# Performance work log

Measured on AMD Instinct MI355X. Metric: run time of the kernel, lower is better.

The kernel has to match this reference:

```python
import jax, jax.numpy as jnp
import numpy as np

B, HT, WD, DIM = 8, 128, 128, 512
NUM_HEADS = 8
HEAD_DIM = DIM // NUM_HEADS
K = 7  # kernel_size
R = K // 2


def setup_inputs() -> dict:
    key = jax.random.key(0)
    k1, k2 = jax.random.split(key)
    x = jax.random.normal(k1, (B, HT, WD, DIM), dtype=jnp.float32)
    # nn.Linear(dim, 2*dim, bias=False); stored as [in, out] so y = x @ W_qk
    W_qk = jax.random.normal(k2, (DIM, 2 * DIM), dtype=jnp.float32) * (DIM ** -0.5)
    return {"x": x, "W_qk": W_qk}


def reference(x, W_qk):
    Bsz, H, W, C = x.shape
    scale = HEAD_DIM ** -0.5
    # qk projection -> [B,H,W,2,heads,head_dim]
    qk = (x @ W_qk).reshape(Bsz, H, W, 2, NUM_HEADS, HEAD_DIM)
    q = qk[..., 0, :, :] * scale          # [B,H,W,hd,d]
    kk = qk[..., 1, :, :]                 # [B,H,W,hd,d]
    # NATTEN border handling: window start clamped so the KxK window stays inside.
    starts_i = jnp.clip(jnp.arange(H) - R, 0, H - K)  # [H]
    starts_j = jnp.clip(jnp.arange(W) - R, 0, W - K)  # [W]
    attn = []
    for ki in range(K):
        k_row = kk[:, starts_i + ki]          # [B,H,W,hd,d] (gather rows)
        for kj in range(K):
            k_n = k_row[:, :, starts_j + kj]  # [B,H,W,hd,d] (gather cols)
            attn.append(jnp.einsum('bhwnd,bhwnd->bhwn', q, k_n))
    attn = jnp.stack(attn, axis=-1)           # [B,H,W,hd,K*K]
    return jnp.transpose(attn, (0, 3, 1, 2, 4))  # [B,hd,H,W,K*K]
```

## Files before the change

### kernel.cpp

```cpp
#include <hip/hip_runtime.h>

typedef __attribute__((ext_vector_type(8))) short short8;
typedef __attribute__((ext_vector_type(4))) float floatx4;

__device__ __forceinline__ unsigned short f2bf(float f) {
  union { float f; unsigned u; } x; x.f = f;
  unsigned u = x.u + 0x7fffu + ((x.u >> 16) & 1u);
  return (unsigned short)(u >> 16);
}

__device__ __forceinline__ void gload_lds16(const void* g, void* l) {
  __builtin_amdgcn_global_load_lds(
      (const __attribute__((address_space(1))) unsigned int*)g,
      (__attribute__((address_space(3))) unsigned int*)l, 16, 0, 0);
}


__global__ __launch_bounds__(256) void cvt_x(const float4* __restrict__ x,
                                             uint2* __restrict__ o) {
  size_t idx = (size_t)blockIdx.x * 256 + threadIdx.x;
  float4 v = x[idx];
  uint2 r;
  r.x = (unsigned)f2bf(v.x) | ((unsigned)f2bf(v.y) << 16);
  r.y = (unsigned)f2bf(v.z) | ((unsigned)f2bf(v.w) << 16);
  o[idx] = r;
}

__global__ __launch_bounds__(256) void cvt_w(const float* __restrict__ w,
                                             unsigned short* __restrict__ wt) {
  int tid = blockIdx.x * 256 + threadIdx.x;
  int n = tid >> 9, k = tid & 511;
  float v = w[k * 1024 + n];
  if (n < 512) v *= 0.125f;
  wt[tid] = f2bf(v);
}

__global__ __launch_bounds__(512, 2) void gemm_bt(const unsigned short* __restrict__ A,
                                                  const unsigned short* __restrict__ Bt,
                                                  unsigned short* __restrict__ C) {
  __shared__ __align__(16) unsigned short lds_a[4][8192];
  __shared__ __align__(16) unsigned short lds_b[4][8192];

  const int t = threadIdx.x;
  const int bid = blockIdx.x;
  const int wg = (bid & 7) * 256 + (bid >> 3);
  const int mtile = wg >> 2;
  const int ntile = wg & 3;
  const int m0 = mtile * 256, n0 = ntile * 256;
  const int wave = t >> 6, lane = t & 63;
  const int wr = wave >> 2, wc = wave & 3;
  const int kg = lane >> 4, rr = lane & 15;

  const unsigned short* aP[2];
  const unsigned short* bP[2];
#pragma unroll
  for (int l = 0; l < 2; ++l) {
    int S = t + l * 512, kgrp = S >> 8, row = S & 255;
    aP[l] = &A[(size_t)(m0 + row) * 512 + kgrp * 8];
    bP[l] = &Bt[(size_t)(n0 + row) * 512 + kgrp * 8];
  }

#pragma unroll
  for (int tt = 0; tt < 3; ++tt)
#pragma unroll
    for (int l = 0; l < 2; ++l) {
      gload_lds16(aP[l] + tt * 32, &lds_a[tt][(t + l * 512) * 8]);
      gload_lds16(bP[l] + tt * 32, &lds_b[tt][(t + l * 512) * 8]);
    }

  floatx4 acc[8][4] = {};

#pragma unroll
  for (int kt = 0; kt < 16; ++kt) {
    const int cur = kt & 3;
    if (kt <= 13)
      asm volatile("s_waitcnt vmcnt(8)\n\ts_barrier" ::: "memory");
    else if (kt == 14)
      asm volatile("s_waitcnt vmcnt(4)\n\ts_barrier" ::: "memory");
    else
      asm volatile("s_waitcnt vmcnt(0)\n\ts_barrier" ::: "memory");

    short8 af[8], bf[4];
#pragma unroll
    for (int i = 0; i < 4; ++i)
      af[i] = *(const short8*)&lds_a[cur][(kg * 256 + wr * 128 + i * 16 + rr) * 8];
#pragma unroll
    for (int j = 0; j < 4; ++j)
      bf[j] = *(const short8*)&lds_b[cur][(kg * 256 + wc * 64 + j * 16 + rr) * 8];
    if (kt <= 12) {
      const int nb = (kt + 3) & 3, k0n = (kt + 3) * 32;
#pragma unroll
      for (int l = 0; l < 2; ++l)
        gload_lds16(aP[l] + k0n, &lds_a[nb][(t + l * 512) * 8]);
    }
    asm volatile("s_barrier" ::: "memory");
    __builtin_amdgcn_s_setprio(1);
#pragma unroll
    for (int i = 0; i < 4; ++i)
#pragma unroll
      for (int j = 0; j < 4; ++j)
        acc[i][j] = __builtin_amdgcn_mfma_f32_16x16x32_bf16(af[i], bf[j], acc[i][j], 0, 0, 0);
    __builtin_amdgcn_s_setprio(0);
    asm volatile("s_barrier" ::: "memory");

#pragma unroll
    for (int i = 4; i < 8; ++i)
      af[i] = *(const short8*)&lds_a[cur][(kg * 256 + wr * 128 + i * 16 + rr) * 8];
    if (kt <= 12) {
      const int nb = (kt + 3) & 3, k0n = (kt + 3) * 32;
#pragma unroll
      for (int l = 0; l < 2; ++l)
        gload_lds16(bP[l] + k0n, &lds_b[nb][(t + l * 512) * 8]);
    }
    asm volatile("s_barrier" ::: "memory");
    __builtin_amdgcn_s_setprio(1);
#pragma unroll
    for (int i = 4; i < 8; ++i)
#pragma unroll
      for (int j = 0; j < 4; ++j)
        acc[i][j] = __builtin_amdgcn_mfma_f32_16x16x32_bf16(af[i], bf[j], acc[i][j], 0, 0, 0);
    __builtin_amdgcn_s_setprio(0);
    asm volatile("s_barrier" ::: "memory");
  }

  __syncthreads();
  unsigned short* cst = (wave < 4) ? &lds_a[wave][0] : &lds_b[wave - 4][0];
#pragma unroll
  for (int i = 0; i < 8; ++i)
#pragma unroll
    for (int j = 0; j < 4; ++j)
#pragma unroll
      for (int r = 0; r < 4; ++r)
        cst[(i * 16 + kg * 4 + r) * 64 + j * 16 + rr] = f2bf(acc[i][j][r]);
  asm volatile("s_waitcnt lgkmcnt(0)" ::: "memory");
  {
    unsigned short* Cg = C + (size_t)(m0 + wr * 128) * 1024 + n0 + wc * 64;
#pragma unroll
    for (int p = 0; p < 16; ++p) {
      int idx = p * 64 + lane;
      int lr = idx >> 3, g8 = idx & 7;
      uint4 v = *(const uint4*)&cst[lr * 64 + g8 * 8];
      *(uint4*)&Cg[(size_t)lr * 1024 + g8 * 8] = v;
    }
  }
}

__global__ __launch_bounds__(256) void attn_mfma(const unsigned short* __restrict__ QK,
                                                 float* __restrict__ out) {
  __shared__ __align__(16) unsigned short q_lds[128 * 64];
  __shared__ __align__(16) unsigned short k_lds[2][128 * 64];
  __shared__ __align__(16) float out_lds[128 * 49];

  const int t = threadIdx.x;
  const int bid = blockIdx.x;
  const int wg = (bid & 7) * 1024 + (bid >> 3);
  const int i = wg & 127;
  const int h = (wg >> 7) & 7;
  const int b = wg >> 10;
  const int wave = t >> 6, lane = t & 63;
  const int kg = lane >> 4, rr = lane & 15;
  const int ri = min(max(i - 3, 0), 121);

  const unsigned short* qbase = QK + ((size_t)(b * 128 + i) * 128) * 1024 + h * 64;
#pragma unroll
  for (int s = 0; s < 4; ++s) {
    int S = t + s * 256;
    int j = S >> 3, pg = S & 7, lg = pg ^ (j & 7);
    gload_lds16(qbase + (size_t)j * 1024 + lg * 8, &q_lds[S * 8]);
  }
#pragma unroll
  for (int kt = 0; kt < 2; ++kt) {
    const unsigned short* kb = QK + ((size_t)(b * 128 + ri + kt) * 128) * 1024 + 512 + h * 64;
#pragma unroll
    for (int s = 0; s < 4; ++s) {
      int S = t + s * 256;
      int c = S >> 3, pg = S & 7, lg = pg ^ (c & 7);
      gload_lds16(kb + (size_t)c * 1024 + lg * 8, &k_lds[kt][S * 8]);
    }
  }

  asm volatile("s_waitcnt vmcnt(8)\n\ts_barrier" ::: "memory");

  short8 af[2][2];
#pragma unroll
  for (int jt2 = 0; jt2 < 2; ++jt2) {
    int row = (wave * 2 + jt2) * 16 + rr;
#pragma unroll
    for (int ks = 0; ks < 2; ++ks) {
      int lg = ks * 4 + kg;
      af[jt2][ks] = *(const short8*)&q_lds[(row * 8 + (lg ^ (row & 7))) * 8];
    }
  }

#pragma unroll
  for (int ki = 0; ki < 7; ++ki) {
    if (ki < 6)
      asm volatile("s_waitcnt vmcnt(4)\n\ts_barrier" ::: "memory");
    else
      asm volatile("s_waitcnt vmcnt(0)\n\ts_barrier" ::: "memory");

    const unsigned short* kbuf = k_lds[ki & 1];

#pragma unroll
    for (int jt2 = 0; jt2 < 2; ++jt2) {
      const int j0 = (wave * 2 + jt2) * 16;
      const int cb = min(max(j0 - 3, 0), 121);
      const int c0 = min(cb + rr, 127);
      const int c1 = min(cb + 16 + rr, 127);
      floatx4 acc0 = {0.f, 0.f, 0.f, 0.f}, acc1 = {0.f, 0.f, 0.f, 0.f};
      __builtin_amdgcn_s_setprio(1);
#pragma unroll
      for (int ks = 0; ks < 2; ++ks) {
        int lg = ks * 4 + kg;
        short8 b0 = *(const short8*)&kbuf[(c0 * 8 + (lg ^ (c0 & 7))) * 8];
        short8 b1 = *(const short8*)&kbuf[(c1 * 8 + (lg ^ (c1 & 7))) * 8];
        acc0 = __builtin_amdgcn_mfma_f32_16x16x32_bf16(af[jt2][ks], b0, acc0, 0, 0, 0);
        acc1 = __builtin_amdgcn_mfma_f32_16x16x32_bf16(af[jt2][ks], b1, acc1, 0, 0, 0);
      }
      __builtin_amdgcn_s_setprio(0);
#pragma unroll
      for (int r = 0; r < 4; ++r) {
        int p = j0 + kg * 4 + r;
        int relc = min(max(p - 3, 0), 121) - cb;
        int k0a = rr - relc;
        if ((unsigned)k0a < 7u) out_lds[p * 49 + ki * 7 + k0a] = acc0[r];
        int k1a = 16 + rr - relc;
        if ((unsigned)k1a < 7u) out_lds[p * 49 + ki * 7 + k1a] = acc1[r];
      }
    }

    asm volatile("s_barrier" ::: "memory");
    if (ki + 2 <= 6) {
      const unsigned short* kb =
          QK + ((size_t)(b * 128 + ri + ki + 2) * 128) * 1024 + 512 + h * 64;
#pragma unroll
      for (int s = 0; s < 4; ++s) {
        int S = t + s * 256;
        int c = S >> 3, pg = S & 7, lg = pg ^ (c & 7);
        gload_lds16(kb + (size_t)c * 1024 + lg * 8, &k_lds[ki & 1][S * 8]);
      }
    }
  }

  __syncthreads();
  const uint4* src = (const uint4*)out_lds;
  uint4* dst = (uint4*)(out + ((size_t)(b * 8 + h) * 16384 + (size_t)i * 128) * 49);
  for (int s = t; s < 1568; s += 256) dst[s] = src[s];
}

extern "C" void kernel_launch(void* const* d_in, const int* in_sizes, int n_in,
                              void* d_out, int out_size, void* d_ws, size_t ws_size,
                              hipStream_t stream) {
  const float* x = (const float*)d_in[0];
  const float* w = (const float*)d_in[1];
  float* out = (float*)d_out;

  unsigned short* xb = (unsigned short*)d_ws;
  unsigned short* wt = xb + 67108864;
  unsigned short* qk = wt + 524288;

  cvt_x<<<65536, 256, 0, stream>>>((const float4*)x, (uint2*)xb);
  cvt_w<<<2048, 256, 0, stream>>>(w, wt);
  gemm_bt<<<2048, 512, 0, stream>>>(xb, wt, qk);
  attn_mfma<<<8192, 256, 0, stream>>>(qk, out);
}
```

Baseline: 798.0 us.

## Process two query rows per attention block to share K-row loads

Each attention workgroup now handles two adjacent query rows with 512 threads, split into two groups of four waves. The K rows are streamed once through a double buffer over eight iterations, and each wave group uses only the seven rows that fall in its own window. This cuts the redundant global loads of K rows shared by neighbouring query rows, since each row was previously loaded seven times. In exchange LDS use roughly doubles, which lowers occupancy, and in some iterations one wave group sits idle.

```diff
diff --git a/kernel.cpp b/kernel.cpp
--- a/kernel.cpp
+++ b/kernel.cpp
@@ -145,107 +145,116 @@
   }
 }
 
-__global__ __launch_bounds__(256) void attn_mfma(const unsigned short* __restrict__ QK,
+__global__ __launch_bounds__(512) void attn_mfma(const unsigned short* __restrict__ QK,
                                                  float* __restrict__ out) {
-  __shared__ __align__(16) unsigned short q_lds[128 * 64];
+  __shared__ __align__(16) unsigned short q_lds[2][128 * 64];
   __shared__ __align__(16) unsigned short k_lds[2][128 * 64];
-  __shared__ __align__(16) float out_lds[128 * 49];
+  __shared__ __align__(16) float out_lds[2][128 * 49];
 
   const int t = threadIdx.x;
   const int bid = blockIdx.x;
-  const int wg = (bid & 7) * 1024 + (bid >> 3);
-  const int i = wg & 127;
-  const int h = (wg >> 7) & 7;
-  const int b = wg >> 10;
+  const int wg = (bid & 7) * 512 + (bid >> 3);
+  const int ridx = wg & 63;
+  const int h = (wg >> 6) & 7;
+  const int b = wg >> 9;
+  const int i0 = ridx * 2;
   const int wave = t >> 6, lane = t & 63;
+  const int iw = wave >> 2, ws = wave & 3;
   const int kg = lane >> 4, rr = lane & 15;
-  const int ri = min(max(i - 3, 0), 121);
-
-  const unsigned short* qbase = QK + ((size_t)(b * 128 + i) * 128) * 1024 + h * 64;
+  const int cr0 = min(max(i0 - 3, 0), 121);
+  const int off1 = min(max(i0 - 2, 0), 121) - cr0;
+  const int myoff = iw ? off1 : 0;
+
 #pragma unroll
   for (int s = 0; s < 4; ++s) {
-    int S = t + s * 256;
-    int j = S >> 3, pg = S & 7, lg = pg ^ (j & 7);
-    gload_lds16(qbase + (size_t)j * 1024 + lg * 8, &q_lds[S * 8]);
+    int S = t + s * 512;
+    int qr = S >> 10, W = S & 1023;
+    int j = W >> 3, pg = W & 7, lg = pg ^ (j & 7);
+    const unsigned short* qb = QK + ((size_t)((b * 128 + i0 + qr) * 128)) * 1024 + h * 64;
+    gload_lds16(qb + (size_t)j * 1024 + lg * 8, &q_lds[qr][W * 8]);
   }
 #pragma unroll
   for (int kt = 0; kt < 2; ++kt) {
-    const unsigned short* kb = QK + ((size_t)(b * 128 + ri + kt) * 128) * 1024 + 512 + h * 64;
-#pragma unroll
-    for (int s = 0; s < 4; ++s) {
-      int S = t + s * 256;
+    int krow = min(cr0 + kt, 127);
+    const unsigned short* kb = QK + ((size_t)((b * 128 + krow) * 128)) * 1024 + 512 + h * 64;
+#pragma unroll
+    for (int s = 0; s < 2; ++s) {
+      int S = t + s * 512;
       int c = S >> 3, pg = S & 7, lg = pg ^ (c & 7);
       gload_lds16(kb + (size_t)c * 1024 + lg * 8, &k_lds[kt][S * 8]);
     }
   }
 
-  asm volatile("s_waitcnt vmcnt(8)\n\ts_barrier" ::: "memory");
+  asm volatile("s_waitcnt vmcnt(4)\n\ts_barrier" ::: "memory");
 
   short8 af[2][2];
 #pragma unroll
   for (int jt2 = 0; jt2 < 2; ++jt2) {
-    int row = (wave * 2 + jt2) * 16 + rr;
+    int row = (ws * 2 + jt2) * 16 + rr;
 #pragma unroll
     for (int ks = 0; ks < 2; ++ks) {
       int lg = ks * 4 + kg;
-      af[jt2][ks] = *(const short8*)&q_lds[(row * 8 + (lg ^ (row & 7))) * 8];
-    }
-  }
-
-#pragma unroll
-  for (int ki = 0; ki < 7; ++ki) {
-    if (ki < 6)
-      asm volatile("s_waitcnt vmcnt(4)\n\ts_barrier" ::: "memory");
+      af[jt2][ks] = *(const short8*)&q_lds[iw][(row * 8 + (lg ^ (row & 7))) * 8];
+    }
+  }
+
+#pragma unroll
+  for (int kt = 0; kt < 8; ++kt) {
+    if (kt < 7)
+      asm volatile("s_waitcnt vmcnt(2)\n\ts_barrier" ::: "memory");
     else
       asm volatile("s_waitcnt vmcnt(0)\n\ts_barrier" ::: "memory");
 
-    const unsigned short* kbuf = k_lds[ki & 1];
-
-#pragma unroll
-    for (int jt2 = 0; jt2 < 2; ++jt2) {
-      const int j0 = (wave * 2 + jt2) * 16;
-      const int cb = min(max(j0 - 3, 0), 121);
-      const int c0 = min(cb + rr, 127);
-      const int c1 = min(cb + 16 + rr, 127);
-      floatx4 acc0 = {0.f, 0.f, 0.f, 0.f}, acc1 = {0.f, 0.f, 0.f, 0.f};
-      __builtin_amdgcn_s_setprio(1);
-#pragma unroll
-      for (int ks = 0; ks < 2; ++ks) {
-        int lg = ks * 4 + kg;
-        short8 b0 = *(const short8*)&kbuf[(c0 * 8 + (lg ^ (c0 & 7))) * 8];
-        short8 b1 = *(const short8*)&kbuf[(c1 * 8 + (lg ^ (c1 & 7))) * 8];
-        acc0 = __builtin_amdgcn_mfma_f32_16x16x32_bf16(af[jt2][ks], b0, acc0, 0, 0, 0);
-        acc1 = __builtin_amdgcn_mfma_f32_16x16x32_bf16(af[jt2][ks], b1, acc1, 0, 0, 0);
+    const unsigned short* kbuf = k_lds[kt & 1];
+    const int ki = kt - myoff;
+    if (0 <= ki && ki <= 6) {
+#pragma unroll
+      for (int jt2 = 0; jt2 < 2; ++jt2) {
+        const int j0 = (ws * 2 + jt2) * 16;
+        const int cb = min(max(j0 - 3, 0), 121);
+        const int c0 = min(cb + rr, 127);
+        const int c1 = min(cb + 16 + rr, 127);
+        floatx4 acc0 = {0.f, 0.f, 0.f, 0.f}, acc1 = {0.f, 0.f, 0.f, 0.f};
+        __builtin_amdgcn_s_setprio(1);
+#pragma unroll
+        for (int ks = 0; ks < 2; ++ks) {
+          int lg = ks * 4 + kg;
+          short8 b0 = *(const short8*)&kbuf[(c0 * 8 + (lg ^ (c0 & 7))) * 8];
+          short8 b1 = *(const short8*)&kbuf[(c1 * 8 + (lg ^ (c1 & 7))) * 8];
+          acc0 = __builtin_amdgcn_mfma_f32_16x16x32_bf16(af[jt2][ks], b0, acc0, 0, 0, 0);
+          acc1 = __builtin_amdgcn_mfma_f32_16x16x32_bf16(af[jt2][ks], b1, acc1, 0, 0, 0);
+        }
+        __builtin_amdgcn_s_setprio(0);
+#pragma unroll
+        for (int r = 0; r < 4; ++r) {
+          int p = j0 + kg * 4 + r;
+          int relc = min(max(p - 3, 0), 121) - cb;
+          int k0a = rr - relc;
+          if ((unsigned)k0a < 7u) out_lds[iw][p * 49 + ki * 7 + k0a] = acc0[r];
+          int k1a = 16 + rr - relc;
+          if ((unsigned)k1a < 7u) out_lds[iw][p * 49 + ki * 7 + k1a] = acc1[r];
+        }
       }
-      __builtin_amdgcn_s_setprio(0);
-#pragma unroll
-      for (int r = 0; r < 4; ++r) {
-        int p = j0 + kg * 4 + r;
-        int relc = min(max(p - 3, 0), 121) - cb;
-        int k0a = rr - relc;
-        if ((unsigned)k0a < 7u) out_lds[p * 49 + ki * 7 + k0a] = acc0[r];
-        int k1a = 16 + rr - relc;
-        if ((unsigned)k1a < 7u) out_lds[p * 49 + ki * 7 + k1a] = acc1[r];
+    }
+
+    asm volatile("s_barrier" ::: "memory");
+    if (kt <= 5) {
+      int krow = min(cr0 + kt + 2, 127);
+      const unsigned short* kb =
+          QK + ((size_t)((b * 128 + krow) * 128)) * 1024 + 512 + h * 64;
+#pragma unroll
+      for (int s = 0; s < 2; ++s) {
+        int S = t + s * 512;
+        int c = S >> 3, pg = S & 7, lg = pg ^ (c & 7);
+        gload_lds16(kb + (size_t)c * 1024 + lg * 8, &k_lds[kt & 1][S * 8]);
       }
     }
-
-    asm volatile("s_barrier" ::: "memory");
-    if (ki + 2 <= 6) {
-      const unsigned short* kb =
-          QK + ((size_t)(b * 128 + ri + ki + 2) * 128) * 1024 + 512 + h * 64;
-#pragma unroll
-      for (int s = 0; s < 4; ++s) {
-        int S = t + s * 256;
-        int c = S >> 3, pg = S & 7, lg = pg ^ (c & 7);
-        gload_lds16(kb + (size_t)c * 1024 + lg * 8, &k_lds[ki & 1][S * 8]);
-      }
-    }
   }
 
   __syncthreads();
-  const uint4* src = (const uint4*)out_lds;
-  uint4* dst = (uint4*)(out + ((size_t)(b * 8 + h) * 16384 + (size_t)i * 128) * 49);
-  for (int s = t; s < 1568; s += 256) dst[s] = src[s];
+  const uint4* src = (const uint4*)&out_lds[0][0];
+  uint4* dst = (uint4*)(out + ((size_t)((b * 8 + h) * 16384 + i0 * 128)) * 49);
+  for (int s = t; s < 3136; s += 512) dst[s] = src[s];
 }
 
 extern "C" void kernel_launch(void* const* d_in, const int* in_sizes, int n_in,
@@ -262,5 +271,5 @@
   cvt_x<<<65536, 256, 0, stream>>>((const float4*)x, (uint2*)xb);
   cvt_w<<<2048, 256, 0, stream>>>(w, wt);
   gemm_bt<<<2048, 512, 0, stream>>>(xb, wt, qk);
-  attn_mfma<<<8192, 256, 0, stream>>>(qk, out);
-}
+  attn_mfma<<<4096, 512, 0, stream>>>(qk, out);
+}
```

Measured after the change: 822.8 us. 3.1% more time.
